# Kernel tuning notes

Hardware: AMD Instinct MI355X
Metric: run time of the kernel (lower is better)

The kernel has to match this reference:

```python
import jax, jax.numpy as jnp
import numpy as np

M, K, N, G = 2048, 1024, 1024, 64


def _dequant(weight, scale, offset):
    # Ascend antiquant: w_fp = (w_int + offset) * scale, per group g and out-channel n
    return (weight.astype(scale.dtype) + offset[:, None, :]) * scale[:, None, :]  # [G,K,N]


def _grouped_dot(x, w, group_sizes):
    # x:[M,K], w:[G,K,N], group_sizes:[G] (rows of x are contiguous per group)
    if hasattr(jax.lax, "ragged_dot"):
        return jax.lax.ragged_dot(x, w, group_sizes.astype(jnp.int32))
    # fallback for older jax: groups are equal-sized in this setup
    g = w.shape[0]
    m = x.shape[0] // g
    return jnp.einsum('gmk,gkn->gmn', x.reshape(g, m, -1), w).reshape(x.shape[0], -1)


def setup_inputs() -> dict:
    key = jax.random.key(0)
    k1, k2, k3, k4 = jax.random.split(key, 4)
    x = jax.random.normal(k1, (M, K), dtype=jnp.float32)
    weight = jax.random.randint(k2, (G, K, N), -8, 8, dtype=jnp.int32)
    antiquant_scale = jax.random.uniform(k3, (G, N), dtype=jnp.float32, minval=0.005, maxval=0.02)
    antiquant_offset = jax.random.normal(k4, (G, N), dtype=jnp.float32)
    # group_list_type == 0 -> cumulative row counts, last entry == M (equal groups here)
    group_list = (jnp.arange(1, G + 1, dtype=jnp.int64) * (M // G))
    return {
        "x": x,
        "weight": weight,
        "antiquant_scale": antiquant_scale,
        "antiquant_offset": antiquant_offset,
        "group_list": group_list,
        "group_list_type": 0,
    }


def reference(x, weight, antiquant_scale, antiquant_offset, group_list, group_list_type):
    w_fp = _dequant(weight, antiquant_scale, antiquant_offset)  # [G,K,N]
    if group_list_type == 0:  # cumulative -> per-group sizes
        group_sizes = jnp.diff(group_list, prepend=jnp.zeros((1,), group_list.dtype))
    else:  # already per-group counts
        group_sizes = group_list
    return _grouped_dot(x, w_fp, group_sizes)  # [M,N]
```

## Files before the change

### kernel.cpp

```cpp
#include <hip/hip_runtime.h>

constexpr int Mdim = 2048;
constexpr int Kdim = 1024;
constexpr int Ndim = 1024;
constexpr int Gdim = 64;
constexpr int ROWS = 32;

typedef float          f32x16 __attribute__((ext_vector_type(16)));
typedef __bf16         bf16x8 __attribute__((ext_vector_type(8)));
typedef unsigned short u16x4  __attribute__((ext_vector_type(4)));
typedef unsigned short u16x8  __attribute__((ext_vector_type(8)));

static __device__ __forceinline__ unsigned short f2bf_rne(float f) {
  unsigned u = __float_as_uint(f);
  u += 0x7FFFu + ((u >> 16) & 1u);
  return (unsigned short)(u >> 16);
}

__global__ __launch_bounds__(512)
void gmm_wq_kernel(const float* __restrict__ x,
                   const int*   __restrict__ w,
                   const float* __restrict__ scale,
                   const float* __restrict__ offs,
                   const void*  __restrict__ gl_raw,
                   const int*   __restrict__ glt,
                   float*       __restrict__ out)
{
  __shared__ __align__(16) unsigned short xs[ROWS * Kdim];

  const int tid   = threadIdx.x;
  const int blk   = blockIdx.x;
  const int g     = blk >> 2;
  const int nbase = (blk & 3) << 8;

  const int*       gl32 = (const int*)gl_raw;
  const long long* gl64 = (const long long*)gl_raw;
  const bool is64 = (gl32[1] == 0);
  auto glv = [&](int i) -> long long { return is64 ? gl64[i] : (long long)gl32[i]; };
  int row_start, rows;
  if (glt[0] == 0) {
    long long prev = (g == 0) ? 0 : glv(g - 1);
    row_start = (int)prev;
    rows      = (int)(glv(g) - prev);
  } else {
    long long s = 0;
    for (int i = 0; i < g; ++i) s += glv(i);
    row_start = (int)s;
    rows      = (int)glv(g);
  }
  rows = (rows > ROWS) ? ROWS : rows;

  {
    const int r   = tid >> 4;
    const int c16 = tid & 15;
    const bool valid = (r < rows);
    const float4* xr = (const float4*)(x + (size_t)(row_start + r) * Kdim);
    const int swz = (r & 7) << 4;
    char* base = (char*)xs + r * (Kdim * 2);
    #pragma unroll
    for (int it = 0; it < 16; ++it) {
      const int c4 = c16 + it * 16;
      float4 v = make_float4(0.f, 0.f, 0.f, 0.f);
      if (valid) v = xr[c4];
      u16x4 h;
      h.x = f2bf_rne(v.x); h.y = f2bf_rne(v.y);
      h.z = f2bf_rne(v.z); h.w = f2bf_rne(v.w);
      *(u16x4*)(base + ((c4 * 8) ^ swz)) = h;
    }
  }
  __syncthreads();

  const int lane  = tid & 63;
  const int wave  = tid >> 6;
  const int n0    = nbase + wave * 32;
  const int nlane = lane & 31;
  const int khalf = lane >> 5;

  const int* wg   = w + (size_t)g * Kdim * Ndim;
  const int  voff = n0 + nlane + khalf * 8 * Ndim;

  const int abase = nlane * (Kdim * 2) + khalf * 16;
  const int axor  = (nlane & 7) << 4;
  const char* xsb = (const char*)xs;

  f32x16 acc, rs;
  #pragma unroll
  for (int i = 0; i < 16; ++i) { acc[i] = 0.f; rs[i] = 0.f; }
  bf16x8 ones;
  #pragma unroll
  for (int e = 0; e < 8; ++e) ones[e] = (__bf16)1.0f;

  auto loadW = [&](int kk, int (&d)[8]) {
    const int* p = wg + (size_t)(kk * 16) * Ndim + voff;
    #pragma unroll
    for (int e = 0; e < 8; ++e) d[e] = p[(size_t)e * Ndim];
  };
  auto cvtW = [&](const int (&s)[8]) -> bf16x8 {
    u16x8 r;
    #pragma unroll
    for (int e = 0; e < 8; ++e)
      r[e] = (unsigned short)(__float_as_uint((float)s[e]) >> 16);
    return __builtin_bit_cast(bf16x8, r);
  };
  auto ldsA = [&](int kk) -> bf16x8 {
    return *(const bf16x8*)(xsb + ((abase + kk * 32) ^ axor));
  };

  int Wa[8], Wb[8], Wc[8];
  loadW(0, Wa); loadW(1, Wb); loadW(2, Wc);

  for (int kk = 0; kk < 63; kk += 3) {
    {
      bf16x8 b = cvtW(Wa);
      if (kk + 3 < 64) loadW(kk + 3, Wa);
      bf16x8 a = ldsA(kk);
      acc = __builtin_amdgcn_mfma_f32_32x32x16_bf16(a, b,    acc, 0, 0, 0);
      rs  = __builtin_amdgcn_mfma_f32_32x32x16_bf16(a, ones, rs,  0, 0, 0);
    }
    {
      bf16x8 b = cvtW(Wb);
      if (kk + 4 < 64) loadW(kk + 4, Wb);
      bf16x8 a = ldsA(kk + 1);
      acc = __builtin_amdgcn_mfma_f32_32x32x16_bf16(a, b,    acc, 0, 0, 0);
      rs  = __builtin_amdgcn_mfma_f32_32x32x16_bf16(a, ones, rs,  0, 0, 0);
    }
    {
      bf16x8 b = cvtW(Wc);
      if (kk + 5 < 64) loadW(kk + 5, Wc);
      bf16x8 a = ldsA(kk + 2);
      acc = __builtin_amdgcn_mfma_f32_32x32x16_bf16(a, b,    acc, 0, 0, 0);
      rs  = __builtin_amdgcn_mfma_f32_32x32x16_bf16(a, ones, rs,  0, 0, 0);
    }
  }
  {
    bf16x8 b = cvtW(Wa);
    bf16x8 a = ldsA(63);
    acc = __builtin_amdgcn_mfma_f32_32x32x16_bf16(a, b,    acc, 0, 0, 0);
    rs  = __builtin_amdgcn_mfma_f32_32x32x16_bf16(a, ones, rs,  0, 0, 0);
  }

  const int col = n0 + nlane;
  const float sc = scale[g * Ndim + col];
  const float of = offs [g * Ndim + col];
  #pragma unroll
  for (int r = 0; r < 16; ++r) {
    const int rl = (r & 3) + 8 * (r >> 2) + 4 * khalf;
    if (rl < rows)
      out[(size_t)(row_start + rl) * Ndim + col] = sc * (acc[r] + of * rs[r]);
  }
}

extern "C" void kernel_launch(void* const* d_in, const int* in_sizes, int n_in,
                              void* d_out, int out_size, void* d_ws, size_t ws_size,
                              hipStream_t stream) {
  const float* x   = (const float*)d_in[0];
  const int*   w   = (const int*)d_in[1];
  const float* sc  = (const float*)d_in[2];
  const float* of  = (const float*)d_in[3];
  const void*  gl  = d_in[4];
  const int*   glt = (const int*)d_in[5];
  float*       out = (float*)d_out;

  hipLaunchKernelGGL(gmm_wq_kernel, dim3(Gdim * 4), dim3(512), 0, stream,
                     x, w, sc, of, gl, glt, out);
}
```

Baseline: 54.84 us.

## Compute row sums during x staging instead of ones-MFMA; remap blocks across groups

Drops the second MFMA per k-step that multiplied x by a ones vector to get row sums. Instead, each row's sum of bf16-rounded values is computed while x is staged into LDS and reduced with shuffles into a shared array. This halves the matrix-core work and frees the rs accumulator registers. Blocks are also remapped so consecutive block IDs touch different groups, and weight addresses are precomputed as byte offsets. The per-row sum is summed in a different order than the MFMA did, so rounding can differ slightly.

```diff
diff --git a/kernel.cpp b/kernel.cpp
--- a/kernel.cpp
+++ b/kernel.cpp
@@ -1,10 +1,10 @@
 #include <hip/hip_runtime.h>
 
-constexpr int Mdim = 2048;
 constexpr int Kdim = 1024;
 constexpr int Ndim = 1024;
 constexpr int Gdim = 64;
 constexpr int ROWS = 32;
+constexpr size_t KSTEP_BYTES = 16ull * Ndim * 4;
 
 typedef float          f32x16 __attribute__((ext_vector_type(16)));
 typedef __bf16         bf16x8 __attribute__((ext_vector_type(8)));
@@ -27,11 +27,13 @@
                    float*       __restrict__ out)
 {
   __shared__ __align__(16) unsigned short xs[ROWS * Kdim];
+  __shared__ float xsum[ROWS];
 
-  const int tid   = threadIdx.x;
-  const int blk   = blockIdx.x;
-  const int g     = blk >> 2;
-  const int nbase = (blk & 3) << 8;
+  const int tid  = threadIdx.x;
+  const int b    = blockIdx.x;
+  const int slot = b >> 3;
+  const int g     = (b & 7) * 8 + (slot >> 2);
+  const int nbase = (slot & 3) << 8;
 
   const int*       gl32 = (const int*)gl_raw;
   const long long* gl64 = (const long long*)gl_raw;
@@ -57,6 +59,7 @@
     const float4* xr = (const float4*)(x + (size_t)(row_start + r) * Kdim);
     const int swz = (r & 7) << 4;
     char* base = (char*)xs + r * (Kdim * 2);
+    float psum = 0.f;
     #pragma unroll
     for (int it = 0; it < 16; ++it) {
       const int c4 = c16 + it * 16;
@@ -66,7 +69,14 @@
       h.x = f2bf_rne(v.x); h.y = f2bf_rne(v.y);
       h.z = f2bf_rne(v.z); h.w = f2bf_rne(v.w);
       *(u16x4*)(base + ((c4 * 8) ^ swz)) = h;
+      psum += __uint_as_float((unsigned)h.x << 16)
+            + __uint_as_float((unsigned)h.y << 16)
+            + __uint_as_float((unsigned)h.z << 16)
+            + __uint_as_float((unsigned)h.w << 16);
     }
+    #pragma unroll
+    for (int m = 8; m >= 1; m >>= 1) psum += __shfl_xor(psum, m);
+    if (c16 == 0) xsum[r] = psum;
   }
   __syncthreads();
 
@@ -76,24 +86,23 @@
   const int nlane = lane & 31;
   const int khalf = lane >> 5;
 
-  const int* wg   = w + (size_t)g * Kdim * Ndim;
-  const int  voff = n0 + nlane + khalf * 8 * Ndim;
+  const char* wbase = (const char*)w + (size_t)g * Kdim * Ndim * 4;
+  int woff[8];
+  #pragma unroll
+  for (int e = 0; e < 8; ++e)
+    woff[e] = ((khalf * 8 + e) * Ndim + n0 + nlane) * 4;
 
   const int abase = nlane * (Kdim * 2) + khalf * 16;
   const int axor  = (nlane & 7) << 4;
   const char* xsb = (const char*)xs;
 
-  f32x16 acc, rs;
+  f32x16 acc;
   #pragma unroll
-  for (int i = 0; i < 16; ++i) { acc[i] = 0.f; rs[i] = 0.f; }
-  bf16x8 ones;
-  #pragma unroll
-  for (int e = 0; e < 8; ++e) ones[e] = (__bf16)1.0f;
+  for (int i = 0; i < 16; ++i) acc[i] = 0.f;
 
-  auto loadW = [&](int kk, int (&d)[8]) {
-    const int* p = wg + (size_t)(kk * 16) * Ndim + voff;
+  auto loadW = [&](const char* p, int (&d)[8]) {
     #pragma unroll
-    for (int e = 0; e < 8; ++e) d[e] = p[(size_t)e * Ndim];
+    for (int e = 0; e < 8; ++e) d[e] = *(const int*)(p + woff[e]);
   };
   auto cvtW = [&](const int (&s)[8]) -> bf16x8 {
     u16x8 r;
@@ -107,36 +116,31 @@
   };
 
   int Wa[8], Wb[8], Wc[8];
-  loadW(0, Wa); loadW(1, Wb); loadW(2, Wc);
+  loadW(wbase,                   Wa);
+  loadW(wbase +     KSTEP_BYTES, Wb);
+  loadW(wbase + 2 * KSTEP_BYTES, Wc);
 
   for (int kk = 0; kk < 63; kk += 3) {
+    const char* pf = wbase + (size_t)(kk + 3) * KSTEP_BYTES;
     {
-      bf16x8 b = cvtW(Wa);
-      if (kk + 3 < 64) loadW(kk + 3, Wa);
-      bf16x8 a = ldsA(kk);
-      acc = __builtin_amdgcn_mfma_f32_32x32x16_bf16(a, b,    acc, 0, 0, 0);
-      rs  = __builtin_amdgcn_mfma_f32_32x32x16_bf16(a, ones, rs,  0, 0, 0);
+      bf16x8 bfr = cvtW(Wa);
+      if (kk + 3 < 64) loadW(pf, Wa);
+      acc = __builtin_amdgcn_mfma_f32_32x32x16_bf16(ldsA(kk), bfr, acc, 0, 0, 0);
     }
     {
-      bf16x8 b = cvtW(Wb);
-      if (kk + 4 < 64) loadW(kk + 4, Wb);
-      bf16x8 a = ldsA(kk + 1);
-      acc = __builtin_amdgcn_mfma_f32_32x32x16_bf16(a, b,    acc, 0, 0, 0);
-      rs  = __builtin_amdgcn_mfma_f32_32x32x16_bf16(a, ones, rs,  0, 0, 0);
+      bf16x8 bfr = cvtW(Wb);
+      if (kk + 4 < 64) loadW(pf + KSTEP_BYTES, Wb);
+      acc = __builtin_amdgcn_mfma_f32_32x32x16_bf16(ldsA(kk + 1), bfr, acc, 0, 0, 0);
     }
     {
-      bf16x8 b = cvtW(Wc);
-      if (kk + 5 < 64) loadW(kk + 5, Wc);
-      bf16x8 a = ldsA(kk + 2);
-      acc = __builtin_amdgcn_mfma_f32_32x32x16_bf16(a, b,    acc, 0, 0, 0);
-      rs  = __builtin_amdgcn_mfma_f32_32x32x16_bf16(a, ones, rs,  0, 0, 0);
+      bf16x8 bfr = cvtW(Wc);
+      if (kk + 5 < 64) loadW(pf + 2 * KSTEP_BYTES, Wc);
+      acc = __builtin_amdgcn_mfma_f32_32x32x16_bf16(ldsA(kk + 2), bfr, acc, 0, 0, 0);
     }
   }
   {
-    bf16x8 b = cvtW(Wa);
-    bf16x8 a = ldsA(63);
-    acc = __builtin_amdgcn_mfma_f32_32x32x16_bf16(a, b,    acc, 0, 0, 0);
-    rs  = __builtin_amdgcn_mfma_f32_32x32x16_bf16(a, ones, rs,  0, 0, 0);
+    bf16x8 bfr = cvtW(Wa);
+    acc = __builtin_amdgcn_mfma_f32_32x32x16_bf16(ldsA(63), bfr, acc, 0, 0, 0);
   }
 
   const int col = n0 + nlane;
@@ -146,7 +150,7 @@
   for (int r = 0; r < 16; ++r) {
     const int rl = (r & 3) + 8 * (r >> 2) + 4 * khalf;
     if (rl < rows)
-      out[(size_t)(row_start + rl) * Ndim + col] = sc * (acc[r] + of * rs[r]);
+      out[(size_t)(row_start + rl) * Ndim + col] = sc * (acc[r] + of * xsum[rl]);
   }
 }
 
```

Result: no change. 54.65 us (-0.3%).
